# Optimization experiments

Measured on AMD Instinct MI355X. Metric: run time of the kernel, lower is better.

Reference implementation:

```python
import jax, jax.numpy as jnp
import numpy as np

B = 8192
IN = 2048
H = 2048


def setup_inputs() -> dict:
    key = jax.random.key(0)
    ks = jax.random.split(key, 6)
    stdv = 1.0 / np.sqrt(H)
    return {
        "x": jax.random.normal(ks[0], (B, IN), dtype=jnp.float32),
        "h_prev": jax.random.normal(ks[1], (B, H), dtype=jnp.float32),
        "c_prev": jax.random.normal(ks[2], (B, H), dtype=jnp.float32),
        "weight_ih": jax.random.normal(ks[3], (4 * H, IN), dtype=jnp.float32) * stdv,
        "weight_hh": jax.random.normal(ks[4], (4 * H, H), dtype=jnp.float32) * stdv,
        "bias": jax.random.normal(ks[5], (4 * H,), dtype=jnp.float32) * stdv,
    }


def reference(x, h_prev, c_prev, weight_ih, weight_hh, bias):
    # gates: [B, 4H] = x @ W_ih^T + h_prev @ W_hh^T + b
    gates = x @ weight_ih.T + h_prev @ weight_hh.T + bias
    i, f, j, o = jnp.split(gates, 4, axis=1)
    i = jax.nn.sigmoid(i)
    f = jax.nn.sigmoid(f)
    o = jax.nn.sigmoid(o)
    j = jnp.tanh(j)
    # cap_input_gate=True: input gate capped by (1 - f)
    c = f * c_prev + jnp.minimum(1.0 - f, i) * j
    h = o * jnp.tanh(c)
    return (h, c)
```

## Files before the change

### kernel.cpp

```cpp
#include <hip/hip_runtime.h>

#define DEVI __device__ __forceinline__

typedef __attribute__((ext_vector_type(8))) __bf16 bf16x8;
typedef __attribute__((ext_vector_type(4))) float floatx4;

constexpr int Bsz = 8192;
constexpr int Hd  = 2048;
constexpr int INd = 2048;
constexpr int N1  = Bsz * INd;

DEVI unsigned short f2bf_rne(float f) {
  unsigned int u = __float_as_uint(f);
  u += 0x7FFFu + ((u >> 16) & 1u);
  return (unsigned short)(u >> 16);
}

__global__ void cvt4(const float* __restrict__ s0, const float* __restrict__ s1,
                     const float* __restrict__ s2, const float* __restrict__ s3,
                     unsigned short* __restrict__ dst) {
  const float* src = (blockIdx.y == 0) ? s0 : (blockIdx.y == 1) ? s1
                   : (blockIdx.y == 2) ? s2 : s3;
  unsigned short* out = dst + (size_t)blockIdx.y * N1;
  const int nv = N1 / 4;
  for (int i = blockIdx.x * blockDim.x + threadIdx.x; i < nv;
       i += gridDim.x * blockDim.x) {
    float4 v = ((const float4*)src)[i];
    ushort4 o;
    o.x = f2bf_rne(v.x); o.y = f2bf_rne(v.y);
    o.z = f2bf_rne(v.z); o.w = f2bf_rne(v.w);
    ((ushort4*)out)[i] = o;
  }
}

DEVI void gload_lds16(const void* g, void* l) {
  __builtin_amdgcn_global_load_lds(
      (const __attribute__((address_space(1))) void*)g,
      (__attribute__((address_space(3))) void*)l, 16, 0, 0);
}

DEVI float sigm(float x) { return 1.0f / (1.0f + __expf(-x)); }

__global__ __launch_bounds__(512, 2) void lstm_gemm(
    const unsigned short* __restrict__ ws,
    const float* __restrict__ bias,
    const float* __restrict__ c_prev,
    float* __restrict__ out_h,
    float* __restrict__ out_c) {
  __shared__ __align__(16) unsigned short sm[4 * 256 * 64];
  char* smc = (char*)sm;

  const unsigned short* xb  = ws;
  const unsigned short* hb  = ws + (size_t)N1;
  const unsigned short* wih = ws + (size_t)2 * N1;
  const unsigned short* whh = ws + (size_t)3 * N1;

  const int tid  = threadIdx.x;
  const int lane = tid & 63;
  const int wid  = tid >> 6;
  const int wm   = wid >> 2, wn = wid & 3;
  const int lr   = lane & 15, lk = lane >> 4;
  const int lr8  = lane >> 3;
  const int swc  = ((lane & 7) ^ lr8) * 8;

  const int wg = blockIdx.x;
  const int x8 = wg & 7;
  const int lc = wg >> 3;
  const int bc = (x8 & 3) * 8 + (lc & 7);
  const int rb = ((x8 >> 2) * 16 + (lc >> 3)) * 256;

  unsigned int aOff[2][2], bOff[2][2];
#pragma unroll
  for (int h = 0; h < 2; ++h)
#pragma unroll
    for (int j = 0; j < 2; ++j) {
      const int arow = rb + h * 128 + j * 64 + wid * 8 + lr8;
      aOff[h][j] = (unsigned)arow * 2048u + (unsigned)swc;
      const int c  = h * 128 + j * 64 + wid * 8 + lr8;
      const int cf = c >> 4, ce = c & 15;
      const int gate = (cf & 1) | ((cf >> 2) & 2);
      const int hch  = (cf >> 1) & 3;
      const int brow = gate * 2048 + bc * 64 + hch * 16 + ce;
      bOff[h][j] = (unsigned)brow * 2048u + (unsigned)swc;
    }

  floatx4 acc[2][4][2][2];
#pragma unroll
  for (int a = 0; a < 2; ++a)
#pragma unroll
    for (int b = 0; b < 4; ++b)
#pragma unroll
      for (int c = 0; c < 2; ++c)
#pragma unroll
        for (int d = 0; d < 2; ++d)
          acc[a][b][c][d] = (floatx4){0.f, 0.f, 0.f, 0.f};

#define STAGE_A(ts, h) {                                                      \
    const int bs_ = (ts) & 1;                                                 \
    const unsigned short* s_ = (((ts) < 32) ? xb : hb) + (((ts) & 31) * 64);  \
    gload_lds16(s_ + aOff[h][0], smc + bs_ * 32768 + ((h) * 128 + wid * 8) * 128);        \
    gload_lds16(s_ + aOff[h][1], smc + bs_ * 32768 + ((h) * 128 + 64 + wid * 8) * 128); }
#define STAGE_B(ts, h) {                                                      \
    const int bs_ = (ts) & 1;                                                 \
    const unsigned short* s_ = (((ts) < 32) ? wih : whh) + (((ts) & 31) * 64);\
    gload_lds16(s_ + bOff[h][0], smc + 65536 + bs_ * 32768 + ((h) * 128 + wid * 8) * 128);        \
    gload_lds16(s_ + bOff[h][1], smc + 65536 + bs_ * 32768 + ((h) * 128 + 64 + wid * 8) * 128); }

#define LDA(DST, QM)                                                          \
  _Pragma("unroll") for (int mr = 0; mr < 4; ++mr)                            \
    _Pragma("unroll") for (int s = 0; s < 2; ++s) {                           \
      const int row  = (QM) * 128 + wm * 64 + mr * 16 + lr;                   \
      const int phys = (s * 4 + lk) ^ (row & 7);                              \
      DST[mr][s] = *(const bf16x8*)(Ab + row * 128 + phys * 16); }
#define LDB(DST, QN)                                                          \
  _Pragma("unroll") for (int nc = 0; nc < 2; ++nc)                            \
    _Pragma("unroll") for (int s = 0; s < 2; ++s) {                           \
      const int row  = ((QN) * 8 + wn * 2 + nc) * 16 + lr;                    \
      const int phys = (s * 4 + lk) ^ (row & 7);                              \
      DST[nc][s] = *(const bf16x8*)(Bb + row * 128 + phys * 16); }
#define MFMA16(QM, QN, AF, BG)                                                \
  __builtin_amdgcn_s_setprio(1);                                              \
  _Pragma("unroll") for (int mr = 0; mr < 4; ++mr)                            \
    _Pragma("unroll") for (int nc = 0; nc < 2; ++nc)                          \
      _Pragma("unroll") for (int s = 0; s < 2; ++s)                           \
        acc[QM][mr][QN][nc] = __builtin_amdgcn_mfma_f32_16x16x32_bf16(        \
            AF[mr][s], BG[nc][s], acc[QM][mr][QN][nc], 0, 0, 0);              \
  __builtin_amdgcn_s_setprio(0);
#define BAR  asm volatile("s_barrier" ::: "memory")
#define VM4  asm volatile("s_waitcnt vmcnt(4)" ::: "memory")
#define VM0  asm volatile("s_waitcnt vmcnt(0)" ::: "memory")
#define NOP  (void)0

#define KTILE(BETA, S1, S2a, S2b, S3, W4) {                                   \
    const char* Ab = smc + (BETA) * 32768;                                    \
    const char* Bb = smc + 65536 + (BETA) * 32768;                            \
    bf16x8 afA[4][2], afB[4][2], bg0[2][2], bg1[2][2];                        \
    LDA(afA, 0); LDB(bg0, 0); LDA(afB, 1); LDB(bg1, 1);                       \
    S1; S2a;                                                                  \
    MFMA16(0, 0, afA, bg0);                                                   \
    MFMA16(1, 0, afB, bg0); BAR;                                              \
    S2b; S3;                                                                  \
    MFMA16(1, 1, afB, bg1);                                                   \
    MFMA16(0, 1, afA, bg1); W4; BAR;                                          \
  }

  STAGE_A(0, 0); STAGE_B(0, 0); STAGE_A(0, 1); STAGE_B(0, 1);
  STAGE_B(1, 0); STAGE_A(1, 1);
  VM0;
  BAR;

  for (int u = 0; u < 31; ++u) {
    const int t0 = 2 * u;
    KTILE(0, STAGE_A(t0 + 1, 0), STAGE_B(t0 + 1, 1),
          STAGE_B(t0 + 2, 0), STAGE_A(t0 + 2, 1), VM4);
    KTILE(1, STAGE_A(t0 + 2, 0), STAGE_B(t0 + 2, 1),
          STAGE_B(t0 + 3, 0), STAGE_A(t0 + 3, 1), VM4);
  }
  KTILE(0, STAGE_A(63, 0), STAGE_B(63, 1), NOP, NOP, VM0);
  KTILE(1, NOP, NOP, NOP, NOP, NOP);

  const int hcol = bc * 64 + wn * 16 + lr;
  const float b_i = bias[hcol];
  const float b_f = bias[2048 + hcol];
  const float b_j = bias[4096 + hcol];
  const float b_o = bias[6144 + hcol];
#pragma unroll
  for (int qm = 0; qm < 2; ++qm)
#pragma unroll
    for (int mr = 0; mr < 4; ++mr)
#pragma unroll
      for (int r = 0; r < 4; ++r) {
        const int row = rb + qm * 128 + wm * 64 + mr * 16 + lk * 4 + r;
        const float gi = acc[qm][mr][0][0][r] + b_i;
        const float gf = acc[qm][mr][0][1][r] + b_f;
        const float gj = acc[qm][mr][1][0][r] + b_j;
        const float go = acc[qm][mr][1][1][r] + b_o;
        const float iv = sigm(gi);
        const float fv = sigm(gf);
        const float jv = tanhf(gj);
        const float ov = sigm(go);
        const size_t idx = (size_t)row * 2048 + hcol;
        const float cp = c_prev[idx];
        const float cv = fv * cp + fminf(1.0f - fv, iv) * jv;
        out_h[idx] = ov * tanhf(cv);
        out_c[idx] = cv;
      }
}

extern "C" void kernel_launch(void* const* d_in, const int* in_sizes, int n_in,
                              void* d_out, int out_size, void* d_ws, size_t ws_size,
                              hipStream_t stream) {
  const float* x      = (const float*)d_in[0];
  const float* h_prev = (const float*)d_in[1];
  const float* c_prev = (const float*)d_in[2];
  const float* w_ih   = (const float*)d_in[3];
  const float* w_hh   = (const float*)d_in[4];
  const float* bias   = (const float*)d_in[5];

  float* out_h = (float*)d_out;
  float* out_c = out_h + (size_t)Bsz * Hd;
  unsigned short* wsb = (unsigned short*)d_ws;

  dim3 cgrid(2048, 4);
  cvt4<<<cgrid, 256, 0, stream>>>(x, h_prev, w_ih, w_hh, wsb);

  lstm_gemm<<<1024, 512, 0, stream>>>(wsb, bias, c_prev, out_h, out_c);
}
```

Before: 569.0 us.

## Interleave LDS fragment loads with MFMAs, precompute LDS pointers, use fast tanh

Precomputes the per-lane swizzled LDS base pointers so fragment addressing reduces to constant offsets. It also reorders each k-tile so A/B fragment loads for later quadrants are issued between MFMA groups instead of all upfront, overlapping LDS reads with matrix math and lowering peak register use. The epilogue's tanhf is replaced by an exp-based formula. The reordering risks new LDS/barrier hazards, and the fast tanh trades some accuracy for speed.

```diff
diff --git a/kernel.cpp b/kernel.cpp
--- a/kernel.cpp
+++ b/kernel.cpp
@@ -40,6 +40,7 @@
 }
 
 DEVI float sigm(float x) { return 1.0f / (1.0f + __expf(-x)); }
+DEVI float tanh_fast(float x) { return 1.0f - 2.0f / (1.0f + __expf(2.0f * x)); }
 
 __global__ __launch_bounds__(512, 2) void lstm_gemm(
     const unsigned short* __restrict__ ws,
@@ -84,6 +85,18 @@
       bOff[h][j] = (unsigned)brow * 2048u + (unsigned)swc;
     }
 
+  const int rA = lr & 7;
+  const char* pA[2][2];
+  const char* pB[2][2];
+#pragma unroll
+  for (int be = 0; be < 2; ++be)
+#pragma unroll
+    for (int s = 0; s < 2; ++s) {
+      const int phys = (s * 4 + lk) ^ rA;
+      pA[be][s] = smc + be * 32768 + wm * 8192 + lr * 128 + phys * 16;
+      pB[be][s] = smc + 65536 + be * 32768 + wn * 4096 + lr * 128 + phys * 16;
+    }
+
   floatx4 acc[2][4][2][2];
 #pragma unroll
   for (int a = 0; a < 2; ++a)
@@ -106,18 +119,14 @@
     gload_lds16(s_ + bOff[h][0], smc + 65536 + bs_ * 32768 + ((h) * 128 + wid * 8) * 128);        \
     gload_lds16(s_ + bOff[h][1], smc + 65536 + bs_ * 32768 + ((h) * 128 + 64 + wid * 8) * 128); }
 
-#define LDA(DST, QM)                                                          \
+#define LDA(DST, BETA, QM)                                                    \
   _Pragma("unroll") for (int mr = 0; mr < 4; ++mr)                            \
-    _Pragma("unroll") for (int s = 0; s < 2; ++s) {                           \
-      const int row  = (QM) * 128 + wm * 64 + mr * 16 + lr;                   \
-      const int phys = (s * 4 + lk) ^ (row & 7);                              \
-      DST[mr][s] = *(const bf16x8*)(Ab + row * 128 + phys * 16); }
-#define LDB(DST, QN)                                                          \
+    _Pragma("unroll") for (int s = 0; s < 2; ++s)                             \
+      DST[mr][s] = *(const bf16x8*)(pA[BETA][s] + ((QM) * 16384 + mr * 2048));
+#define LDB(DST, BETA, QN)                                                    \
   _Pragma("unroll") for (int nc = 0; nc < 2; ++nc)                            \
-    _Pragma("unroll") for (int s = 0; s < 2; ++s) {                           \
-      const int row  = ((QN) * 8 + wn * 2 + nc) * 16 + lr;                    \
-      const int phys = (s * 4 + lk) ^ (row & 7);                              \
-      DST[nc][s] = *(const bf16x8*)(Bb + row * 128 + phys * 16); }
+    _Pragma("unroll") for (int s = 0; s < 2; ++s)                             \
+      DST[nc][s] = *(const bf16x8*)(pB[BETA][s] + ((QN) * 16384 + nc * 2048));
 #define MFMA16(QM, QN, AF, BG)                                                \
   __builtin_amdgcn_s_setprio(1);                                              \
   _Pragma("unroll") for (int mr = 0; mr < 4; ++mr)                            \
@@ -132,14 +141,12 @@
 #define NOP  (void)0
 
 #define KTILE(BETA, S1, S2a, S2b, S3, W4) {                                   \
-    const char* Ab = smc + (BETA) * 32768;                                    \
-    const char* Bb = smc + 65536 + (BETA) * 32768;                            \
     bf16x8 afA[4][2], afB[4][2], bg0[2][2], bg1[2][2];                        \
-    LDA(afA, 0); LDB(bg0, 0); LDA(afB, 1); LDB(bg1, 1);                       \
-    S1; S2a;                                                                  \
+    LDA(afA, BETA, 0); LDB(bg0, BETA, 0); S1;                                 \
     MFMA16(0, 0, afA, bg0);                                                   \
+    LDA(afB, BETA, 1); S2a;                                                   \
     MFMA16(1, 0, afB, bg0); BAR;                                              \
-    S2b; S3;                                                                  \
+    LDB(bg1, BETA, 1); S2b; S3;                                               \
     MFMA16(1, 1, afB, bg1);                                                   \
     MFMA16(0, 1, afA, bg1); W4; BAR;                                          \
   }
@@ -177,12 +184,12 @@
         const float go = acc[qm][mr][1][1][r] + b_o;
         const float iv = sigm(gi);
         const float fv = sigm(gf);
-        const float jv = tanhf(gj);
+        const float jv = tanh_fast(gj);
         const float ov = sigm(go);
         const size_t idx = (size_t)row * 2048 + hcol;
         const float cp = c_prev[idx];
         const float cv = fv * cp + fminf(1.0f - fv, iv) * jv;
-        out_h[idx] = ov * tanhf(cv);
+        out_h[idx] = ov * tanh_fast(cv);
         out_c[idx] = cv;
       }
 }
```

After: 515.2 us. -9.5%, faster.
